# Optimization experiments

Measured on AMD Instinct MI355X. Metric: run time of the kernel, lower is better.

Reference implementation:

```python
import jax, jax.numpy as jnp
import numpy as np

EMBED_DIM = 1024
N_HEADS = 16
HEAD_SIZE = EMBED_DIM // N_HEADS
SEQ_LEN = 2048
BATCH = 4


def setup_inputs() -> dict:
    key = jax.random.key(0)
    ks = jax.random.split(key, 9)
    s = 0.02
    d = EMBED_DIM
    return {
        "x": jax.random.normal(ks[0], (BATCH, SEQ_LEN, d), dtype=jnp.float32),
        "wq": jax.random.normal(ks[1], (d, d), dtype=jnp.float32) * s,
        "bq": jnp.zeros((d,), dtype=jnp.float32),
        "wk": jax.random.normal(ks[2], (d, d), dtype=jnp.float32) * s,
        "bk": jnp.zeros((d,), dtype=jnp.float32),
        "wv": jax.random.normal(ks[3], (d, d), dtype=jnp.float32) * s,
        "bv": jnp.zeros((d,), dtype=jnp.float32),
        "wo": jax.random.normal(ks[4], (d, d), dtype=jnp.float32) * s,
        "bo": jnp.zeros((d,), dtype=jnp.float32),
    }


def reference(x, wq, bq, wk, bk, wv, bv, wo, bo):
    b, t, c = x.shape
    h, hs = N_HEADS, HEAD_SIZE
    scale = hs ** -0.5
    # projections (torch Linear: x @ W^T + b); here weights stored as [in, out]
    q = (x @ wq + bq).reshape(b, t, h, hs).transpose(0, 2, 1, 3)  # [b,h,t,hs]
    k = (x @ wk + bk).reshape(b, t, h, hs).transpose(0, 2, 1, 3)
    v = (x @ wv + bv).reshape(b, t, h, hs).transpose(0, 2, 1, 3)
    scores = jnp.einsum('bhqd,bhkd->bhqk', q, k) * scale  # [b,h,t,t]
    causal = jnp.tril(jnp.ones((t, t), dtype=bool))
    scores = jnp.where(causal, scores, -jnp.inf)
    probs = jax.nn.softmax(scores, axis=-1)
    attn = jnp.einsum('bhqk,bhkd->bhqd', probs, v)  # [b,h,t,hs]
    attn = attn.transpose(0, 2, 1, 3).reshape(b, t, c)
    return attn @ wo + bo
```

## Files before the change

kernel.cpp:

```cpp
#include <hip/hip_runtime.h>

#define EMBED 1024
#define NH 16
#define HS 64
#define SEQT 2048
#define NB 4

typedef unsigned short u16;
typedef unsigned int u32;
typedef __attribute__((ext_vector_type(8))) __bf16 bf16x8;
typedef __attribute__((ext_vector_type(4))) float f32x4;
typedef __attribute__((ext_vector_type(4))) unsigned short u16x4;

__device__ __forceinline__ u16 f2bf(float f) {
  __bf16 h = (__bf16)f;
  return __builtin_bit_cast(u16, h);
}

__device__ __forceinline__ void gload_lds16(const void* g, void* l) {
  __builtin_amdgcn_global_load_lds((const __attribute__((address_space(1))) void*)g,
                                   (__attribute__((address_space(3))) void*)l, 16, 0, 0);
}

#define MFMA16(a, b, c) __builtin_amdgcn_mfma_f32_16x16x32_bf16(a, b, c, 0, 0, 0)
#define LDS_FENCE() asm volatile("" ::: "memory")

__global__ void cvt_x(const float* __restrict__ in, u16* __restrict__ out) {
  int i = (blockIdx.x * 256 + threadIdx.x) * 4;
  float4 v = *(const float4*)(in + i);
  u16x4 o;
  o[0] = f2bf(v.x); o[1] = f2bf(v.y); o[2] = f2bf(v.z); o[3] = f2bf(v.w);
  *(u16x4*)(out + i) = o;
}

__global__ void wtrans(const float* __restrict__ w0, const float* __restrict__ w1,
                       const float* __restrict__ w2, const float* __restrict__ w3,
                       u16* __restrict__ t0, u16* __restrict__ t1,
                       u16* __restrict__ t2, u16* __restrict__ t3) {
  __shared__ float tile[32][33];
  const float* w; u16* t;
  switch (blockIdx.z) {
    case 0: w = w0; t = t0; break;
    case 1: w = w1; t = t1; break;
    case 2: w = w2; t = t2; break;
    default: w = w3; t = t3; break;
  }
  int n0 = blockIdx.x * 32, k0 = blockIdx.y * 32;
  int tx = threadIdx.x, ty = threadIdx.y;
#pragma unroll
  for (int r = 0; r < 4; ++r)
    tile[ty + r * 8][tx] = w[(size_t)(k0 + ty + r * 8) * EMBED + n0 + tx];
  __syncthreads();
#pragma unroll
  for (int r = 0; r < 4; ++r)
    t[(size_t)(n0 + ty + r * 8) * EMBED + k0 + tx] = f2bf(tile[tx][ty + r * 8]);
}

template <int BM, int MREP>
__device__ __forceinline__ void gemm_core(
    const u16* __restrict__ A, const u16* __restrict__ Bt, int m0, int n0,
    u16 (&As)[2][BM * 64], u16 (&Bs)[2][256 * 64],
    f32x4 (&acc)[MREP][4], int lane, int wid) {
  const int tid = wid * 64 + lane;
  const int lr = lane & 15, lg = lane >> 4;
  const int arow = tid >> 3;
  const int csw = ((tid & 7) ^ (arow & 7)) * 8;
  const int ldst = arow * 64 + (tid & 7) * 8;
  const int wrb = (wid >> 2) * (BM / 2);
  const int wcb = (wid & 3) * 64;
  const u16* Aa = A + (size_t)m0 * EMBED;
  const u16* Bb = Bt + (size_t)n0 * EMBED;

  auto stage = [&](const u16* src, u16* dst, int j, int k0) {
    gload_lds16(src + (size_t)(arow + 64 * j) * EMBED + k0 + csw, dst + j * 4096 + ldst);
  };
  auto rd = [&](const u16* buf, int row, int kk) -> bf16x8 {
    return *(const bf16x8*)(buf + row * 64 + (((kk * 4 + lg) ^ (lr & 7)) * 8));
  };

#pragma unroll
  for (int j = 0; j < BM / 64; ++j) stage(Aa, As[0], j, 0);
#pragma unroll
  for (int j = 0; j < 4; ++j) stage(Bb, Bs[0], j, 0);

  for (int t = 0; t < 16; ++t) {
    const int kn = (t + 1) * 64;
    u16* Ac = (t & 1) ? As[1] : As[0];
    u16* Bc = (t & 1) ? Bs[1] : Bs[0];
    u16* An = (t & 1) ? As[0] : As[1];
    u16* Bn = (t & 1) ? Bs[0] : Bs[1];
    const bool pf = (t < 15);

    bf16x8 af[MREP / 2][2], bf0[2][2], bf1[2][2];

    if (pf) {
      stage(Aa, An, 0, kn);
      if constexpr (BM == 256) {
        stage(Aa, An, 1, kn);
        asm volatile("s_waitcnt vmcnt(2)" ::: "memory");
      } else {
        asm volatile("s_waitcnt vmcnt(1)" ::: "memory");
      }
    } else {
      asm volatile("s_waitcnt vmcnt(0)" ::: "memory");
    }
    __builtin_amdgcn_sched_barrier(0);
    __builtin_amdgcn_s_barrier();
    LDS_FENCE();
#pragma unroll
    for (int mi = 0; mi < MREP / 2; ++mi)
#pragma unroll
      for (int kk = 0; kk < 2; ++kk) af[mi][kk] = rd(Ac, wrb + mi * 16 + lr, kk);
#pragma unroll
    for (int ni = 0; ni < 2; ++ni)
#pragma unroll
      for (int kk = 0; kk < 2; ++kk) bf0[ni][kk] = rd(Bc, wcb + ni * 16 + lr, kk);
    __builtin_amdgcn_s_setprio(1);
#pragma unroll
    for (int mi = 0; mi < MREP / 2; ++mi)
#pragma unroll
      for (int ni = 0; ni < 2; ++ni) {
        acc[mi][ni] = MFMA16(af[mi][0], bf0[ni][0], acc[mi][ni]);
        acc[mi][ni] = MFMA16(af[mi][1], bf0[ni][1], acc[mi][ni]);
      }
    __builtin_amdgcn_s_setprio(0);
    __builtin_amdgcn_s_barrier();
    LDS_FENCE();

    if (pf) {
      if constexpr (BM == 256) { stage(Aa, An, 2, kn); stage(Aa, An, 3, kn); }
      else stage(Aa, An, 1, kn);
    }
#pragma unroll
    for (int ni = 0; ni < 2; ++ni)
#pragma unroll
      for (int kk = 0; kk < 2; ++kk) bf1[ni][kk] = rd(Bc, wcb + (2 + ni) * 16 + lr, kk);
    __builtin_amdgcn_s_setprio(1);
#pragma unroll
    for (int mi = 0; mi < MREP / 2; ++mi)
#pragma unroll
      for (int ni = 0; ni < 2; ++ni) {
        acc[mi][2 + ni] = MFMA16(af[mi][0], bf1[ni][0], acc[mi][2 + ni]);
        acc[mi][2 + ni] = MFMA16(af[mi][1], bf1[ni][1], acc[mi][2 + ni]);
      }
    __builtin_amdgcn_s_setprio(0);
    __builtin_amdgcn_s_barrier();
    LDS_FENCE();

    if (pf) { stage(Bb, Bn, 0, kn); stage(Bb, Bn, 1, kn); }
#pragma unroll
    for (int mi = 0; mi < MREP / 2; ++mi)
#pragma unroll
      for (int kk = 0; kk < 2; ++kk)
        af[mi][kk] = rd(Ac, wrb + (MREP / 2 + mi) * 16 + lr, kk);
    __builtin_amdgcn_s_setprio(1);
#pragma unroll
    for (int mi = 0; mi < MREP / 2; ++mi)
#pragma unroll
      for (int ni = 0; ni < 2; ++ni) {
        acc[MREP / 2 + mi][2 + ni] = MFMA16(af[mi][0], bf1[ni][0], acc[MREP / 2 + mi][2 + ni]);
        acc[MREP / 2 + mi][2 + ni] = MFMA16(af[mi][1], bf1[ni][1], acc[MREP / 2 + mi][2 + ni]);
      }
    __builtin_amdgcn_s_setprio(0);
    __builtin_amdgcn_s_barrier();
    LDS_FENCE();

    if (pf) { stage(Bb, Bn, 2, kn); stage(Bb, Bn, 3, kn); }
    __builtin_amdgcn_s_setprio(1);
#pragma unroll
    for (int mi = 0; mi < MREP / 2; ++mi)
#pragma unroll
      for (int ni = 0; ni < 2; ++ni) {
        acc[MREP / 2 + mi][ni] = MFMA16(af[mi][0], bf0[ni][0], acc[MREP / 2 + mi][ni]);
        acc[MREP / 2 + mi][ni] = MFMA16(af[mi][1], bf0[ni][1], acc[MREP / 2 + mi][ni]);
      }
    __builtin_amdgcn_s_setprio(0);
    __builtin_amdgcn_s_barrier();
    LDS_FENCE();
  }
}

__global__ __launch_bounds__(512, 2) void gemm_qkv(
    const u16* __restrict__ A, const u16* __restrict__ Bt,
    const float* __restrict__ bq, const float* __restrict__ bk, const float* __restrict__ bv,
    u16* __restrict__ qo, u16* __restrict__ ko, u16* __restrict__ vto) {
  __shared__ __align__(16) u16 As[2][256 * 64];
  __shared__ __align__(16) u16 Bs[2][256 * 64];
  const int bid = blockIdx.x;
  const int swz = (bid & 7) * 48 + (bid >> 3);
  const int bm = swz / 12, bn = swz % 12;
  const int m0 = bm * 256, n0 = bn * 256;
  const int lane = threadIdx.x & 63, wid = threadIdx.x >> 6;
  const int lr = lane & 15, lg = lane >> 4;
  const int z = n0 >> 10;
  const float* bias = (z == 0) ? bq : ((z == 1) ? bk : bv);
  const float sc = (z == 0) ? 0.18033688011112042f : 1.0f;

  f32x4 acc[8][4];
  const f32x4 zero = {0.f, 0.f, 0.f, 0.f};
#pragma unroll
  for (int m = 0; m < 8; ++m)
#pragma unroll
    for (int n = 0; n < 4; ++n) acc[m][n] = zero;

  gemm_core<256, 8>(A, Bt, m0, n0, As, Bs, acc, lane, wid);

  const int wrb = (wid >> 2) * 128, wcb = (wid & 3) * 64;
#pragma unroll
  for (int n = 0; n < 4; ++n) {
    int col = n0 + wcb + n * 16 + lr;
    int lcol = col & 1023;
    float bv_ = bias[lcol];
    int h = lcol >> 6, d = lcol & 63;
#pragma unroll
    for (int m = 0; m < 8; ++m) {
      int r0 = m0 + wrb + m * 16 + lg * 4;
      int b_ = r0 >> 11, t_ = r0 & 2047;
      if (z < 2) {
        u16* dst = (z == 0) ? qo : ko;
#pragma unroll
        for (int i = 0; i < 4; ++i)
          dst[(((size_t)(b_ * NH + h)) * SEQT + t_ + i) * HS + d] = f2bf((acc[m][n][i] + bv_) * sc);
      } else {
        u16x4 v;
#pragma unroll
        for (int i = 0; i < 4; ++i) v[i] = f2bf(acc[m][n][i] + bv_);
        *(u16x4*)(vto + (((size_t)(b_ * NH + h)) * HS + d) * SEQT + t_) = v;
      }
    }
  }
}

__global__ __launch_bounds__(512, 2) void gemm_out(
    const u16* __restrict__ A, const u16* __restrict__ wot,
    const float* __restrict__ bo, float* __restrict__ out) {
  __shared__ __align__(16) u16 As[2][128 * 64];
  __shared__ __align__(16) u16 Bs[2][256 * 64];
  const int bid = blockIdx.x;
  const int swz = (bid & 7) * 32 + (bid >> 3);
  const int bm = swz >> 2, bn = swz & 3;
  const int m0 = bm * 128, n0 = bn * 256;
  const int lane = threadIdx.x & 63, wid = threadIdx.x >> 6;
  const int lr = lane & 15, lg = lane >> 4;

  f32x4 acc[4][4];
  const f32x4 zero = {0.f, 0.f, 0.f, 0.f};
#pragma unroll
  for (int m = 0; m < 4; ++m)
#pragma unroll
    for (int n = 0; n < 4; ++n) acc[m][n] = zero;

  gemm_core<128, 4>(A, wot, m0, n0, As, Bs, acc, lane, wid);

  const int wrb = (wid >> 2) * 64, wcb = (wid & 3) * 64;
#pragma unroll
  for (int n = 0; n < 4; ++n) {
    int col = n0 + wcb + n * 16 + lr;
    float bv_ = bo[col];
#pragma unroll
    for (int m = 0; m < 4; ++m) {
      int r0 = m0 + wrb + m * 16 + lg * 4;
#pragma unroll
      for (int i = 0; i < 4; ++i)
        out[(size_t)(r0 + i) * EMBED + col] = acc[m][n][i] + bv_;
    }
  }
}

__global__ __launch_bounds__(256, 3) void flash(
    const u16* __restrict__ q, const u16* __restrict__ k,
    const u16* __restrict__ vt, u16* __restrict__ attnb) {
  __shared__ __align__(16) u16 Ks[2][4096];
  __shared__ __align__(16) u16 Vs[2][4096];
  __shared__ __align__(16) u16 Pl[4][2048];
  const int tid = threadIdx.x, lane = tid & 63, wid = tid >> 6;
  const int lr = lane & 15, lg = lane >> 4;
  const int g = blockIdx.x >> 6, pair = blockIdx.x & 63;
  const int qtile = 15 - g;
  const u16* Qh = q + (size_t)pair * SEQT * HS;
  const u16* Kh = k + (size_t)pair * SEQT * HS;
  const u16* Vh = vt + (size_t)pair * HS * SEQT;

  const int sr0 = wid * 16 + (lane >> 3);
  const int sc0 = (lane & 7) ^ (sr0 & 7);
  const int sr1 = sr0 + 8;
  const int sc1 = (lane & 7) ^ (sr1 & 7);
  const int koff0 = sr0 * 64 + sc0 * 8;
  const int koff1 = sr1 * 64 + sc1 * 8;
  const size_t voff0 = (size_t)sr0 * SEQT + sc0 * 8;
  const size_t voff1 = (size_t)sr1 * SEQT + sc1 * 8;

  auto STAGE = [&](int t, int b) {
    const u16* Kb = Kh + (size_t)t * 4096;
    const u16* Vb = Vh + (size_t)t * 64;
    gload_lds16(Kb + koff0, &Ks[b][wid * 1024]);
    gload_lds16(Kb + koff1, &Ks[b][wid * 1024 + 512]);
    gload_lds16(Vb + voff0, &Vs[b][wid * 1024]);
    gload_lds16(Vb + voff1, &Vs[b][wid * 1024 + 512]);
  };

  const int b_ = pair >> 4, h = pair & 15;
  const int qw = qtile * 128 + wid * 32;

  bf16x8 qf[2][2];
#pragma unroll
  for (int nq = 0; nq < 2; ++nq)
#pragma unroll
    for (int ks = 0; ks < 2; ++ks)
      qf[nq][ks] = *(const bf16x8*)(Qh + (size_t)(qw + nq * 16 + lr) * HS + ks * 32 + lg * 8);

  f32x4 o[2][4];
  const f32x4 zero = {0.f, 0.f, 0.f, 0.f};
#pragma unroll
  for (int mr = 0; mr < 2; ++mr)
#pragma unroll
    for (int nd = 0; nd < 4; ++nd) o[mr][nd] = zero;
  float mrow[2] = {-1e30f, -1e30f}, lrow[2] = {0.f, 0.f};

  const int nt = (qtile + 1) * 2;
  int cur = 0;
  STAGE(0, 0);
  __syncthreads();

  for (int t = 0; t < nt; ++t) {
    if (t + 1 < nt) STAGE(t + 1, cur ^ 1);
    const int k0 = t * 64;

    bf16x8 kf[4][2];
#pragma unroll
    for (int mf = 0; mf < 4; ++mf) {
      const int row = mf * 16 + lr;
#pragma unroll
      for (int ks = 0; ks < 2; ++ks)
        kf[mf][ks] = *(const bf16x8*)(&Ks[cur][row * 64 + ((ks * 4 + lg) ^ (lr & 7)) * 8]);
    }
    f32x4 s[2][4];
    __builtin_amdgcn_s_setprio(1);
#pragma unroll
    for (int nq = 0; nq < 2; ++nq)
#pragma unroll
      for (int mf = 0; mf < 4; ++mf) {
        f32x4 a = zero;
        a = MFMA16(kf[mf][0], qf[nq][0], a);
        a = MFMA16(kf[mf][1], qf[nq][1], a);
        s[nq][mf] = a;
      }
    __builtin_amdgcn_s_setprio(0);
    bf16x8 vf[4][2];
#pragma unroll
    for (int nd = 0; nd < 4; ++nd) {
      const int row = nd * 16 + lr;
#pragma unroll
      for (int ks = 0; ks < 2; ++ks)
        vf[nd][ks] = *(const bf16x8*)(&Vs[cur][row * 64 + ((ks * 4 + lg) ^ (lr & 7)) * 8]);
    }

#pragma unroll
    for (int nq = 0; nq < 2; ++nq) {
      const int qmin = qw + nq * 16;
      if (k0 + 63 > qmin) {
        const int ql = qmin + lr;
#pragma unroll
        for (int mf = 0; mf < 4; ++mf) {
          const int kvb = k0 + mf * 16 + lg * 4;
#pragma unroll
          for (int r = 0; r < 4; ++r)
            if (kvb + r > ql) s[nq][mf][r] = -3.0e38f;
        }
      }
      float t0 = fmaxf(fmaxf(s[nq][0][0], s[nq][0][1]), fmaxf(s[nq][0][2], s[nq][0][3]));
      float t1 = fmaxf(fmaxf(s[nq][1][0], s[nq][1][1]), fmaxf(s[nq][1][2], s[nq][1][3]));
      float t2 = fmaxf(fmaxf(s[nq][2][0], s[nq][2][1]), fmaxf(s[nq][2][2], s[nq][2][3]));
      float t3 = fmaxf(fmaxf(s[nq][3][0], s[nq][3][1]), fmaxf(s[nq][3][2], s[nq][3][3]));
      float mx = fmaxf(fmaxf(t0, t1), fmaxf(t2, t3));
      mx = fmaxf(mx, __shfl_xor(mx, 16, 64));
      mx = fmaxf(mx, __shfl_xor(mx, 32, 64));
      if (__any(mx > mrow[nq] + 8.0f)) {
        const float mn = fmaxf(mrow[nq], mx);
        const float al = exp2f(mrow[nq] - mn);
        mrow[nq] = mn;
        lrow[nq] *= al;
        float ao[4];
#pragma unroll
        for (int r = 0; r < 4; ++r) ao[r] = __shfl(al, lg * 4 + r, 64);
#pragma unroll
        for (int nd = 0; nd < 4; ++nd)
#pragma unroll
          for (int r = 0; r < 4; ++r) o[nq][nd][r] *= ao[r];
      }
      const float mn = mrow[nq];
      float rs = 0.f;
#pragma unroll
      for (int mf = 0; mf < 4; ++mf) {
        u16x4 pk;
#pragma unroll
        for (int r = 0; r < 4; ++r) {
          const float pv = exp2f(s[nq][mf][r] - mn);
          rs += pv;
          pk[r] = f2bf(pv);
        }
        *(u16x4*)(&Pl[wid][(nq * 16 + lr) * 64 +
                           (((2 * mf + (lg >> 1)) ^ (lr & 7)) * 8 + (lg & 1) * 4)]) = pk;
      }
      rs += __shfl_xor(rs, 16, 64);
      rs += __shfl_xor(rs, 32, 64);
      lrow[nq] += rs;
    }

    bf16x8 pa[2][2];
#pragma unroll
    for (int mr = 0; mr < 2; ++mr)
#pragma unroll
      for (int ks = 0; ks < 2; ++ks)
        pa[mr][ks] = *(const bf16x8*)(&Pl[wid][(mr * 16 + lr) * 64 + ((ks * 4 + lg) ^ (lr & 7)) * 8]);
    __builtin_amdgcn_s_setprio(1);
#pragma unroll
    for (int mr = 0; mr < 2; ++mr)
#pragma unroll
      for (int nd = 0; nd < 4; ++nd) {
        o[mr][nd] = MFMA16(pa[mr][0], vf[nd][0], o[mr][nd]);
        o[mr][nd] = MFMA16(pa[mr][1], vf[nd][1], o[mr][nd]);
      }
    __builtin_amdgcn_s_setprio(0);

    __syncthreads();
    cur ^= 1;
  }

#pragma unroll
  for (int mr = 0; mr < 2; ++mr) {
    const float lv = 1.0f / lrow[mr];
    float li[4];
#pragma unroll
    for (int r = 0; r < 4; ++r) li[r] = __shfl(lv, lg * 4 + r, 64);
#pragma unroll
    for (int nd = 0; nd < 4; ++nd) {
      const int d = nd * 16 + lr;
#pragma unroll
      for (int r = 0; r < 4; ++r) {
        const int t_ = qw + mr * 16 + lg * 4 + r;
        attnb[((size_t)(b_ * SEQT + t_)) * EMBED + h * 64 + d] = f2bf(o[mr][nd][r] * li[r]);
      }
    }
  }
}

extern "C" void kernel_launch(void* const* d_in, const int* in_sizes, int n_in,
                              void* d_out, int out_size, void* d_ws, size_t ws_size,
                              hipStream_t stream) {
  const float* x  = (const float*)d_in[0];
  const float* wq = (const float*)d_in[1];
  const float* bq = (const float*)d_in[2];
  const float* wk = (const float*)d_in[3];
  const float* bk = (const float*)d_in[4];
  const float* wv = (const float*)d_in[5];
  const float* bv = (const float*)d_in[6];
  const float* wo = (const float*)d_in[7];
  const float* bo = (const float*)d_in[8];
  float* out = (float*)d_out;

  char* ws = (char*)d_ws;
  const size_t XB = 16777216;
  const size_t WB = 2097152;
  const size_t QB = 16777216;
  u16* xb     = (u16*)(ws);
  u16* wqkvbt = (u16*)(ws + XB);
  u16* wobt   = (u16*)(ws + XB + 3 * WB);
  u16* qb     = (u16*)(ws + XB + 4 * WB);
  u16* kb     = (u16*)(ws + XB + 4 * WB + QB);
  u16* vtb    = (u16*)(ws + XB + 4 * WB + 2 * QB);
  u16* attnb  = (u16*)(ws + XB + 4 * WB + 3 * QB);

  hipLaunchKernelGGL(cvt_x, dim3(8192), dim3(256), 0, stream, x, xb);
  hipLaunchKernelGGL(wtrans, dim3(32, 32, 4), dim3(32, 8), 0, stream,
                     wq, wk, wv, wo,
                     wqkvbt, wqkvbt + 1048576, wqkvbt + 2097152, wobt);
  hipLaunchKernelGGL(gemm_qkv, dim3(384), dim3(512), 0, stream,
                     xb, wqkvbt, bq, bk, bv, qb, kb, vtb);
  hipLaunchKernelGGL(flash, dim3(1024), dim3(256), 0, stream, qb, kb, vtb, attnb);
  hipLaunchKernelGGL(gemm_out, dim3(256), dim3(512), 0, stream, attnb, wobt, bo, out);
}
```

Measured before the change: 280.0 us.

## Restructure GEMM mainloop into k-half phases with fewer barriers and reordered prefetch

The GEMM mainloop now splits each 64-wide k tile into two 32-wide halves and loads all four B fragments at once, instead of splitting the work by column quarters. Global-to-LDS prefetch is reordered so B is staged first and A rows are interleaved. The s_waitcnt vmcnt counts are retuned to match, which cuts the number of workgroup barriers per iteration from four to one or two. The aim is lower barrier and synchronization overhead and better overlap of loads with MFMA work. The risks are higher register pressure from holding more live B fragments, and a subtle ordering hazard if the wait counts do not match the new staging order.

After: 274.8 us. Within noise of the previous version (-1.9%).

```diff
diff --git a/kernel.cpp b/kernel.cpp
--- a/kernel.cpp
+++ b/kernel.cpp
@@ -78,10 +78,14 @@
     return *(const bf16x8*)(buf + row * 64 + (((kk * 4 + lg) ^ (lr & 7)) * 8));
   };
 
-#pragma unroll
-  for (int j = 0; j < BM / 64; ++j) stage(Aa, As[0], j, 0);
-#pragma unroll
-  for (int j = 0; j < 4; ++j) stage(Bb, Bs[0], j, 0);
+  stage(Bb, Bs[0], 0, 0); stage(Bb, Bs[0], 1, 0);
+  stage(Bb, Bs[0], 2, 0); stage(Bb, Bs[0], 3, 0);
+  if constexpr (BM == 256) {
+    stage(Aa, As[0], 0, 0); stage(Aa, As[0], 2, 0);
+    stage(Aa, As[0], 1, 0); stage(Aa, As[0], 3, 0);
+  } else {
+    stage(Aa, As[0], 0, 0); stage(Aa, As[0], 1, 0);
+  }
 
   for (int t = 0; t < 16; ++t) {
     const int kn = (t + 1) * 64;
@@ -91,89 +95,78 @@
     u16* Bn = (t & 1) ? Bs[0] : Bs[1];
     const bool pf = (t < 15);
 
-    bf16x8 af[MREP / 2][2], bf0[2][2], bf1[2][2];
-
-    if (pf) {
-      stage(Aa, An, 0, kn);
-      if constexpr (BM == 256) {
-        stage(Aa, An, 1, kn);
-        asm volatile("s_waitcnt vmcnt(2)" ::: "memory");
-      } else {
-        asm volatile("s_waitcnt vmcnt(1)" ::: "memory");
-      }
+    bf16x8 af[MREP / 2], bf[4];
+
+    if (pf) { stage(Bb, Bn, 0, kn); stage(Bb, Bn, 1, kn); }
+    if constexpr (BM == 256) {
+      if (pf) asm volatile("s_waitcnt vmcnt(4)" ::: "memory");
+      else    asm volatile("s_waitcnt vmcnt(2)" ::: "memory");
     } else {
-      asm volatile("s_waitcnt vmcnt(0)" ::: "memory");
+      if (pf) asm volatile("s_waitcnt vmcnt(2)" ::: "memory");
+      else    asm volatile("s_waitcnt vmcnt(0)" ::: "memory");
     }
     __builtin_amdgcn_sched_barrier(0);
     __builtin_amdgcn_s_barrier();
     LDS_FENCE();
 #pragma unroll
-    for (int mi = 0; mi < MREP / 2; ++mi)
-#pragma unroll
-      for (int kk = 0; kk < 2; ++kk) af[mi][kk] = rd(Ac, wrb + mi * 16 + lr, kk);
-#pragma unroll
-    for (int ni = 0; ni < 2; ++ni)
-#pragma unroll
-      for (int kk = 0; kk < 2; ++kk) bf0[ni][kk] = rd(Bc, wcb + ni * 16 + lr, kk);
-    __builtin_amdgcn_s_setprio(1);
-#pragma unroll
-    for (int mi = 0; mi < MREP / 2; ++mi)
-#pragma unroll
-      for (int ni = 0; ni < 2; ++ni) {
-        acc[mi][ni] = MFMA16(af[mi][0], bf0[ni][0], acc[mi][ni]);
-        acc[mi][ni] = MFMA16(af[mi][1], bf0[ni][1], acc[mi][ni]);
-      }
-    __builtin_amdgcn_s_setprio(0);
-    __builtin_amdgcn_s_barrier();
-    LDS_FENCE();
+    for (int mi = 0; mi < MREP / 2; ++mi) af[mi] = rd(Ac, wrb + mi * 16 + lr, 0);
+#pragma unroll
+    for (int ni = 0; ni < 4; ++ni) bf[ni] = rd(Bc, wcb + ni * 16 + lr, 0);
+    __builtin_amdgcn_s_setprio(1);
+#pragma unroll
+    for (int mi = 0; mi < MREP / 2; ++mi)
+#pragma unroll
+      for (int ni = 0; ni < 4; ++ni)
+        acc[mi][ni] = MFMA16(af[mi], bf[ni], acc[mi][ni]);
+    __builtin_amdgcn_s_setprio(0);
+
+    if (pf) { stage(Bb, Bn, 2, kn); stage(Bb, Bn, 3, kn); }
+    if constexpr (BM == 256) {
+      if (pf) asm volatile("s_waitcnt vmcnt(4)" ::: "memory");
+      else    asm volatile("s_waitcnt vmcnt(0)" ::: "memory");
+      __builtin_amdgcn_sched_barrier(0);
+      __builtin_amdgcn_s_barrier();
+      LDS_FENCE();
+    }
+#pragma unroll
+    for (int mi = 0; mi < MREP / 2; ++mi)
+      af[mi] = rd(Ac, wrb + (MREP / 2 + mi) * 16 + lr, 0);
+    __builtin_amdgcn_s_setprio(1);
+#pragma unroll
+    for (int mi = 0; mi < MREP / 2; ++mi)
+#pragma unroll
+      for (int ni = 0; ni < 4; ++ni)
+        acc[MREP / 2 + mi][ni] = MFMA16(af[mi], bf[ni], acc[MREP / 2 + mi][ni]);
+    __builtin_amdgcn_s_setprio(0);
 
     if (pf) {
-      if constexpr (BM == 256) { stage(Aa, An, 2, kn); stage(Aa, An, 3, kn); }
-      else stage(Aa, An, 1, kn);
-    }
-#pragma unroll
-    for (int ni = 0; ni < 2; ++ni)
-#pragma unroll
-      for (int kk = 0; kk < 2; ++kk) bf1[ni][kk] = rd(Bc, wcb + (2 + ni) * 16 + lr, kk);
-    __builtin_amdgcn_s_setprio(1);
-#pragma unroll
-    for (int mi = 0; mi < MREP / 2; ++mi)
-#pragma unroll
-      for (int ni = 0; ni < 2; ++ni) {
-        acc[mi][2 + ni] = MFMA16(af[mi][0], bf1[ni][0], acc[mi][2 + ni]);
-        acc[mi][2 + ni] = MFMA16(af[mi][1], bf1[ni][1], acc[mi][2 + ni]);
-      }
-    __builtin_amdgcn_s_setprio(0);
-    __builtin_amdgcn_s_barrier();
-    LDS_FENCE();
-
-    if (pf) { stage(Bb, Bn, 0, kn); stage(Bb, Bn, 1, kn); }
-#pragma unroll
-    for (int mi = 0; mi < MREP / 2; ++mi)
-#pragma unroll
-      for (int kk = 0; kk < 2; ++kk)
-        af[mi][kk] = rd(Ac, wrb + (MREP / 2 + mi) * 16 + lr, kk);
-    __builtin_amdgcn_s_setprio(1);
-#pragma unroll
-    for (int mi = 0; mi < MREP / 2; ++mi)
-#pragma unroll
-      for (int ni = 0; ni < 2; ++ni) {
-        acc[MREP / 2 + mi][2 + ni] = MFMA16(af[mi][0], bf1[ni][0], acc[MREP / 2 + mi][2 + ni]);
-        acc[MREP / 2 + mi][2 + ni] = MFMA16(af[mi][1], bf1[ni][1], acc[MREP / 2 + mi][2 + ni]);
-      }
-    __builtin_amdgcn_s_setprio(0);
-    __builtin_amdgcn_s_barrier();
-    LDS_FENCE();
-
-    if (pf) { stage(Bb, Bn, 2, kn); stage(Bb, Bn, 3, kn); }
-    __builtin_amdgcn_s_setprio(1);
-#pragma unroll
-    for (int mi = 0; mi < MREP / 2; ++mi)
-#pragma unroll
-      for (int ni = 0; ni < 2; ++ni) {
-        acc[MREP / 2 + mi][ni] = MFMA16(af[mi][0], bf0[ni][0], acc[MREP / 2 + mi][ni]);
-        acc[MREP / 2 + mi][ni] = MFMA16(af[mi][1], bf0[ni][1], acc[MREP / 2 + mi][ni]);
-      }
+      if constexpr (BM == 256) { stage(Aa, An, 0, kn); stage(Aa, An, 2, kn); }
+      else                     { stage(Aa, An, 0, kn); stage(Aa, An, 1, kn); }
+    }
+#pragma unroll
+    for (int mi = 0; mi < MREP / 2; ++mi) af[mi] = rd(Ac, wrb + mi * 16 + lr, 1);
+#pragma unroll
+    for (int ni = 0; ni < 4; ++ni) bf[ni] = rd(Bc, wcb + ni * 16 + lr, 1);
+    __builtin_amdgcn_s_setprio(1);
+#pragma unroll
+    for (int mi = 0; mi < MREP / 2; ++mi)
+#pragma unroll
+      for (int ni = 0; ni < 4; ++ni)
+        acc[mi][ni] = MFMA16(af[mi], bf[ni], acc[mi][ni]);
+    __builtin_amdgcn_s_setprio(0);
+
+    if (pf) {
+      if constexpr (BM == 256) { stage(Aa, An, 1, kn); stage(Aa, An, 3, kn); }
+    }
+#pragma unroll
+    for (int mi = 0; mi < MREP / 2; ++mi)
+      af[mi] = rd(Ac, wrb + (MREP / 2 + mi) * 16 + lr, 1);
+    __builtin_amdgcn_s_setprio(1);
+#pragma unroll
+    for (int mi = 0; mi < MREP / 2; ++mi)
+#pragma unroll
+      for (int ni = 0; ni < 4; ++ni)
+        acc[MREP / 2 + mi][ni] = MFMA16(af[mi], bf[ni], acc[MREP / 2 + mi][ni]);
     __builtin_amdgcn_s_setprio(0);
     __builtin_amdgcn_s_barrier();
     LDS_FENCE();
```

## Rewrite GEMM core as 8-wave quadrant-phased pipeline with half-tile staging

Applied to the files above, without the earlier changes.

Replaces the templated GEMM main loop with a 256x256 core that splits each wave's output into four quadrants. It streams A and B in 128-row halves across two K-stage buffers, with finer waitcnt and barrier phasing so global-to-LDS loads overlap the MFMA work. The output projection GEMM moves to the same 256x256 tile, halving its grid from 256 to 128 blocks. The intent is to hide load latency and raise MFMA density, at the cost of more barriers and fewer blocks in the output GEMM, which may leave CUs idle.

Measured after the change: 280.5 us. About the same (+0.2%).

```diff
diff --git a/kernel.cpp b/kernel.cpp
--- a/kernel.cpp
+++ b/kernel.cpp
@@ -56,136 +56,163 @@
     t[(size_t)(n0 + ty + r * 8) * EMBED + k0 + tx] = f2bf(tile[tx][ty + r * 8]);
 }
 
-template <int BM, int MREP>
-__device__ __forceinline__ void gemm_core(
-    const u16* __restrict__ A, const u16* __restrict__ Bt, int m0, int n0,
-    u16 (&As)[2][BM * 64], u16 (&Bs)[2][256 * 64],
-    f32x4 (&acc)[MREP][4], int lane, int wid) {
+__device__ __forceinline__ void gemm8_core(
+    const u16* __restrict__ Aa, const u16* __restrict__ Bb,
+    u16 (&As)[2][16384], u16 (&Bs)[2][16384],
+    f32x4 (&acc)[8][4], int lane, int wid) {
   const int tid = wid * 64 + lane;
   const int lr = lane & 15, lg = lane >> 4;
-  const int arow = tid >> 3;
-  const int csw = ((tid & 7) ^ (arow & 7)) * 8;
-  const int ldst = arow * 64 + (tid & 7) * 8;
-  const int wrb = (wid >> 2) * (BM / 2);
-  const int wcb = (wid & 3) * 64;
-  const u16* Aa = A + (size_t)m0 * EMBED;
-  const u16* Bb = Bt + (size_t)n0 * EMBED;
-
-  auto stage = [&](const u16* src, u16* dst, int j, int k0) {
-    gload_lds16(src + (size_t)(arow + 64 * j) * EMBED + k0 + csw, dst + j * 4096 + ldst);
+  const int srow = tid >> 3;
+  const int csw = ((tid & 7) ^ (srow & 7)) * 8;
+  const int arb = (wid >> 2) * 64;
+  const int brb = (wid & 3) * 32;
+
+  auto stageH = [&](const u16* src, u16* buf, int half, int k0) {
+    const u16* s = src + (size_t)(half * 128) * EMBED + k0 + csw;
+    u16* d = buf + half * 8192 + tid * 8;
+    gload_lds16(s + (size_t)srow * EMBED, d);
+    gload_lds16(s + (size_t)(srow + 64) * EMBED, d + 4096);
   };
   auto rd = [&](const u16* buf, int row, int kk) -> bf16x8 {
     return *(const bf16x8*)(buf + row * 64 + (((kk * 4 + lg) ^ (lr & 7)) * 8));
   };
 
-#pragma unroll
-  for (int j = 0; j < BM / 64; ++j) stage(Aa, As[0], j, 0);
-#pragma unroll
-  for (int j = 0; j < 4; ++j) stage(Bb, Bs[0], j, 0);
-
-  for (int t = 0; t < 16; ++t) {
-    const int kn = (t + 1) * 64;
-    u16* Ac = (t & 1) ? As[1] : As[0];
-    u16* Bc = (t & 1) ? Bs[1] : Bs[0];
-    u16* An = (t & 1) ? As[0] : As[1];
-    u16* Bn = (t & 1) ? Bs[0] : Bs[1];
-    const bool pf = (t < 15);
-
-    bf16x8 af[MREP / 2][2], bf0[2][2], bf1[2][2];
-
+  stageH(Aa, As[0], 0, 0); stageH(Bb, Bs[0], 0, 0);
+  stageH(Aa, As[0], 1, 0); stageH(Bb, Bs[0], 1, 0);
+  stageH(Aa, As[1], 0, 64); stageH(Bb, Bs[1], 0, 64);
+  stageH(Aa, As[1], 1, 64);
+  asm volatile("s_waitcnt vmcnt(6)" ::: "memory");
+  __builtin_amdgcn_sched_barrier(0);
+  __builtin_amdgcn_s_barrier();
+  LDS_FENCE();
+
+  bf16x8 af0[4][2], af1[4][2], bf0[2][2], bf1[2][2];
+
+#define PH_TOP(LG8)                                              \
+  do {                                                           \
+    if (LG8) asm volatile("s_waitcnt lgkmcnt(8)" ::: "memory");  \
+    __builtin_amdgcn_sched_barrier(0);                           \
+    __builtin_amdgcn_s_barrier();                                \
+    asm volatile("s_waitcnt lgkmcnt(0)" ::: "memory");           \
+    __builtin_amdgcn_sched_barrier(0);                           \
+  } while (0)
+#define PH_END()                                                 \
+  do { __builtin_amdgcn_s_barrier(); LDS_FENCE(); } while (0)
+#define QUAD(RH, CH, AF, BF)                                     \
+  do {                                                           \
+    __builtin_amdgcn_s_setprio(1);                               \
+    _Pragma("unroll") for (int mi = 0; mi < 4; ++mi)             \
+      _Pragma("unroll") for (int ni = 0; ni < 2; ++ni) {         \
+        acc[(RH)*4+mi][(CH)*2+ni] = MFMA16(AF[mi][0], BF[ni][0], acc[(RH)*4+mi][(CH)*2+ni]); \
+        acc[(RH)*4+mi][(CH)*2+ni] = MFMA16(AF[mi][1], BF[ni][1], acc[(RH)*4+mi][(CH)*2+ni]); \
+      }                                                          \
+    __builtin_amdgcn_s_setprio(0);                               \
+  } while (0)
+
+  for (int it = 0; it < 8; ++it) {
+    const int kv  = it * 128 + 64;
+    const int ku2 = it * 128 + 128;
+    const int kv2 = it * 128 + 192;
+    const bool pf = (it < 7);
+
+#pragma unroll
+    for (int mi = 0; mi < 4; ++mi) {
+      af0[mi][0] = rd(As[0], arb + mi * 16 + lr, 0);
+      af0[mi][1] = rd(As[0], arb + mi * 16 + lr, 1);
+    }
+#pragma unroll
+    for (int ni = 0; ni < 2; ++ni) {
+      bf0[ni][0] = rd(Bs[0], brb + ni * 16 + lr, 0);
+      bf0[ni][1] = rd(Bs[0], brb + ni * 16 + lr, 1);
+    }
+    stageH(Bb, Bs[1], 1, kv);
+    PH_TOP(true);
+    QUAD(0, 0, af0, bf0);
+    PH_END();
+
+#pragma unroll
+    for (int mi = 0; mi < 4; ++mi) {
+      af1[mi][0] = rd(As[0], 128 + arb + mi * 16 + lr, 0);
+      af1[mi][1] = rd(As[0], 128 + arb + mi * 16 + lr, 1);
+    }
+    if (pf) stageH(Aa, As[0], 0, ku2);
+    PH_TOP(false);
+    QUAD(1, 0, af1, bf0);
+    PH_END();
+
+#pragma unroll
+    for (int ni = 0; ni < 2; ++ni) {
+      bf1[ni][0] = rd(Bs[0], 128 + brb + ni * 16 + lr, 0);
+      bf1[ni][1] = rd(Bs[0], 128 + brb + ni * 16 + lr, 1);
+    }
+    if (pf) stageH(Bb, Bs[0], 0, ku2);
+    PH_TOP(false);
+    QUAD(1, 1, af1, bf1);
+    PH_END();
+
+    if (pf) stageH(Aa, As[0], 1, ku2);
+    PH_TOP(false);
+    QUAD(0, 1, af0, bf1);
+    if (pf) asm volatile("s_waitcnt vmcnt(6)" ::: "memory");
+    else    asm volatile("s_waitcnt vmcnt(0)" ::: "memory");
+    __builtin_amdgcn_sched_barrier(0);
+    PH_END();
+
+#pragma unroll
+    for (int mi = 0; mi < 4; ++mi) {
+      af0[mi][0] = rd(As[1], arb + mi * 16 + lr, 0);
+      af0[mi][1] = rd(As[1], arb + mi * 16 + lr, 1);
+    }
+#pragma unroll
+    for (int ni = 0; ni < 2; ++ni) {
+      bf0[ni][0] = rd(Bs[1], brb + ni * 16 + lr, 0);
+      bf0[ni][1] = rd(Bs[1], brb + ni * 16 + lr, 1);
+    }
+    if (pf) stageH(Bb, Bs[0], 1, ku2);
+    PH_TOP(true);
+    QUAD(0, 0, af0, bf0);
+    PH_END();
+
+#pragma unroll
+    for (int mi = 0; mi < 4; ++mi) {
+      af1[mi][0] = rd(As[1], 128 + arb + mi * 16 + lr, 0);
+      af1[mi][1] = rd(As[1], 128 + arb + mi * 16 + lr, 1);
+    }
+    if (pf) stageH(Aa, As[1], 0, kv2);
+    PH_TOP(false);
+    QUAD(1, 0, af1, bf0);
+    PH_END();
+
+#pragma unroll
+    for (int ni = 0; ni < 2; ++ni) {
+      bf1[ni][0] = rd(Bs[1], 128 + brb + ni * 16 + lr, 0);
+      bf1[ni][1] = rd(Bs[1], 128 + brb + ni * 16 + lr, 1);
+    }
+    if (pf) stageH(Bb, Bs[1], 0, kv2);
+    PH_TOP(false);
+    QUAD(1, 1, af1, bf1);
+    PH_END();
+
+    if (pf) stageH(Aa, As[1], 1, kv2);
+    PH_TOP(false);
+    QUAD(0, 1, af0, bf1);
     if (pf) {
-      stage(Aa, An, 0, kn);
-      if constexpr (BM == 256) {
-        stage(Aa, An, 1, kn);
-        asm volatile("s_waitcnt vmcnt(2)" ::: "memory");
-      } else {
-        asm volatile("s_waitcnt vmcnt(1)" ::: "memory");
-      }
-    } else {
-      asm volatile("s_waitcnt vmcnt(0)" ::: "memory");
-    }
-    __builtin_amdgcn_sched_barrier(0);
-    __builtin_amdgcn_s_barrier();
-    LDS_FENCE();
-#pragma unroll
-    for (int mi = 0; mi < MREP / 2; ++mi)
-#pragma unroll
-      for (int kk = 0; kk < 2; ++kk) af[mi][kk] = rd(Ac, wrb + mi * 16 + lr, kk);
-#pragma unroll
-    for (int ni = 0; ni < 2; ++ni)
-#pragma unroll
-      for (int kk = 0; kk < 2; ++kk) bf0[ni][kk] = rd(Bc, wcb + ni * 16 + lr, kk);
-    __builtin_amdgcn_s_setprio(1);
-#pragma unroll
-    for (int mi = 0; mi < MREP / 2; ++mi)
-#pragma unroll
-      for (int ni = 0; ni < 2; ++ni) {
-        acc[mi][ni] = MFMA16(af[mi][0], bf0[ni][0], acc[mi][ni]);
-        acc[mi][ni] = MFMA16(af[mi][1], bf0[ni][1], acc[mi][ni]);
-      }
-    __builtin_amdgcn_s_setprio(0);
-    __builtin_amdgcn_s_barrier();
-    LDS_FENCE();
-
-    if (pf) {
-      if constexpr (BM == 256) { stage(Aa, An, 2, kn); stage(Aa, An, 3, kn); }
-      else stage(Aa, An, 1, kn);
-    }
-#pragma unroll
-    for (int ni = 0; ni < 2; ++ni)
-#pragma unroll
-      for (int kk = 0; kk < 2; ++kk) bf1[ni][kk] = rd(Bc, wcb + (2 + ni) * 16 + lr, kk);
-    __builtin_amdgcn_s_setprio(1);
-#pragma unroll
-    for (int mi = 0; mi < MREP / 2; ++mi)
-#pragma unroll
-      for (int ni = 0; ni < 2; ++ni) {
-        acc[mi][2 + ni] = MFMA16(af[mi][0], bf1[ni][0], acc[mi][2 + ni]);
-        acc[mi][2 + ni] = MFMA16(af[mi][1], bf1[ni][1], acc[mi][2 + ni]);
-      }
-    __builtin_amdgcn_s_setprio(0);
-    __builtin_amdgcn_s_barrier();
-    LDS_FENCE();
-
-    if (pf) { stage(Bb, Bn, 0, kn); stage(Bb, Bn, 1, kn); }
-#pragma unroll
-    for (int mi = 0; mi < MREP / 2; ++mi)
-#pragma unroll
-      for (int kk = 0; kk < 2; ++kk)
-        af[mi][kk] = rd(Ac, wrb + (MREP / 2 + mi) * 16 + lr, kk);
-    __builtin_amdgcn_s_setprio(1);
-#pragma unroll
-    for (int mi = 0; mi < MREP / 2; ++mi)
-#pragma unroll
-      for (int ni = 0; ni < 2; ++ni) {
-        acc[MREP / 2 + mi][2 + ni] = MFMA16(af[mi][0], bf1[ni][0], acc[MREP / 2 + mi][2 + ni]);
-        acc[MREP / 2 + mi][2 + ni] = MFMA16(af[mi][1], bf1[ni][1], acc[MREP / 2 + mi][2 + ni]);
-      }
-    __builtin_amdgcn_s_setprio(0);
-    __builtin_amdgcn_s_barrier();
-    LDS_FENCE();
-
-    if (pf) { stage(Bb, Bn, 2, kn); stage(Bb, Bn, 3, kn); }
-    __builtin_amdgcn_s_setprio(1);
-#pragma unroll
-    for (int mi = 0; mi < MREP / 2; ++mi)
-#pragma unroll
-      for (int ni = 0; ni < 2; ++ni) {
-        acc[MREP / 2 + mi][ni] = MFMA16(af[mi][0], bf0[ni][0], acc[MREP / 2 + mi][ni]);
-        acc[MREP / 2 + mi][ni] = MFMA16(af[mi][1], bf0[ni][1], acc[MREP / 2 + mi][ni]);
-      }
-    __builtin_amdgcn_s_setprio(0);
-    __builtin_amdgcn_s_barrier();
-    LDS_FENCE();
+      asm volatile("s_waitcnt vmcnt(6)" ::: "memory");
+      __builtin_amdgcn_sched_barrier(0);
+      PH_END();
+    }
   }
+#undef PH_TOP
+#undef PH_END
+#undef QUAD
 }
 
 __global__ __launch_bounds__(512, 2) void gemm_qkv(
     const u16* __restrict__ A, const u16* __restrict__ Bt,
     const float* __restrict__ bq, const float* __restrict__ bk, const float* __restrict__ bv,
     u16* __restrict__ qo, u16* __restrict__ ko, u16* __restrict__ vto) {
-  __shared__ __align__(16) u16 As[2][256 * 64];
-  __shared__ __align__(16) u16 Bs[2][256 * 64];
+  __shared__ __align__(16) u16 As[2][16384];
+  __shared__ __align__(16) u16 Bs[2][16384];
   const int bid = blockIdx.x;
   const int swz = (bid & 7) * 48 + (bid >> 3);
   const int bm = swz / 12, bn = swz % 12;
@@ -203,18 +230,17 @@
 #pragma unroll
     for (int n = 0; n < 4; ++n) acc[m][n] = zero;
 
-  gemm_core<256, 8>(A, Bt, m0, n0, As, Bs, acc, lane, wid);
-
-  const int wrb = (wid >> 2) * 128, wcb = (wid & 3) * 64;
+  gemm8_core(A + (size_t)m0 * EMBED, Bt + (size_t)n0 * EMBED, As, Bs, acc, lane, wid);
+
 #pragma unroll
   for (int n = 0; n < 4; ++n) {
-    int col = n0 + wcb + n * 16 + lr;
+    int col = n0 + (n >> 1) * 128 + (wid & 3) * 32 + (n & 1) * 16 + lr;
     int lcol = col & 1023;
     float bv_ = bias[lcol];
     int h = lcol >> 6, d = lcol & 63;
 #pragma unroll
     for (int m = 0; m < 8; ++m) {
-      int r0 = m0 + wrb + m * 16 + lg * 4;
+      int r0 = m0 + (m >> 2) * 128 + (wid >> 2) * 64 + (m & 3) * 16 + lg * 4;
       int b_ = r0 >> 11, t_ = r0 & 2047;
       if (z < 2) {
         u16* dst = (z == 0) ? qo : ko;
@@ -234,32 +260,31 @@
 __global__ __launch_bounds__(512, 2) void gemm_out(
     const u16* __restrict__ A, const u16* __restrict__ wot,
     const float* __restrict__ bo, float* __restrict__ out) {
-  __shared__ __align__(16) u16 As[2][128 * 64];
-  __shared__ __align__(16) u16 Bs[2][256 * 64];
+  __shared__ __align__(16) u16 As[2][16384];
+  __shared__ __align__(16) u16 Bs[2][16384];
   const int bid = blockIdx.x;
-  const int swz = (bid & 7) * 32 + (bid >> 3);
+  const int swz = (bid & 7) * 16 + (bid >> 3);
   const int bm = swz >> 2, bn = swz & 3;
-  const int m0 = bm * 128, n0 = bn * 256;
+  const int m0 = bm * 256, n0 = bn * 256;
   const int lane = threadIdx.x & 63, wid = threadIdx.x >> 6;
   const int lr = lane & 15, lg = lane >> 4;
 
-  f32x4 acc[4][4];
+  f32x4 acc[8][4];
   const f32x4 zero = {0.f, 0.f, 0.f, 0.f};
 #pragma unroll
-  for (int m = 0; m < 4; ++m)
+  for (int m = 0; m < 8; ++m)
 #pragma unroll
     for (int n = 0; n < 4; ++n) acc[m][n] = zero;
 
-  gemm_core<128, 4>(A, wot, m0, n0, As, Bs, acc, lane, wid);
-
-  const int wrb = (wid >> 2) * 64, wcb = (wid & 3) * 64;
+  gemm8_core(A + (size_t)m0 * EMBED, wot + (size_t)n0 * EMBED, As, Bs, acc, lane, wid);
+
 #pragma unroll
   for (int n = 0; n < 4; ++n) {
-    int col = n0 + wcb + n * 16 + lr;
+    int col = n0 + (n >> 1) * 128 + (wid & 3) * 32 + (n & 1) * 16 + lr;
     float bv_ = bo[col];
 #pragma unroll
-    for (int m = 0; m < 4; ++m) {
-      int r0 = m0 + wrb + m * 16 + lg * 4;
+    for (int m = 0; m < 8; ++m) {
+      int r0 = m0 + (m >> 2) * 128 + (wid >> 2) * 64 + (m & 3) * 16 + lg * 4;
 #pragma unroll
       for (int i = 0; i < 4; ++i)
         out[(size_t)(r0 + i) * EMBED + col] = acc[m][n][i] + bv_;
@@ -478,5 +503,5 @@
   hipLaunchKernelGGL(gemm_qkv, dim3(384), dim3(512), 0, stream,
                      xb, wqkvbt, bq, bk, bv, qb, kb, vtb);
   hipLaunchKernelGGL(flash, dim3(1024), dim3(256), 0, stream, qb, kb, vtb, attnb);
-  hipLaunchKernelGGL(gemm_out, dim3(256), dim3(512), 0, stream, attnb, wobt, bo, out);
-}
+  hipLaunchKernelGGL(gemm_out, dim3(128), dim3(512), 0, stream, attnb, wobt, bo, out);
+}
```
